# Kernel optimization log

Hardware: AMD Instinct MI355X
Metric: run time of the kernel (lower is better)

The kernel has to match this reference:

```python
import jax, jax.numpy as jnp
import numpy as np

THETA = 10000.0

def _rope_cos_sin(seq_len, head_dim, dtype=jnp.float32):
    # matches precompute_freqs_cis: freqs over even indices of head_dim
    inv = 1.0 / (THETA ** (jnp.arange(0, head_dim, 2, dtype=jnp.float32) / head_dim))  # [hd/2]
    ang = jnp.arange(seq_len, dtype=jnp.float32)[:, None] * inv[None, :]               # [S, hd/2]
    return jnp.cos(ang).astype(dtype), jnp.sin(ang).astype(dtype)

def _apply_rope(x, cos, sin):
    # x: [b, h, s, d]; pairs are interleaved (d r) with r=2 -> complex (even=real, odd=imag)
    xe = x[..., 0::2]
    xo = x[..., 1::2]
    re = xe * cos - xo * sin
    im = xe * sin + xo * cos
    # interleave back: [..., d/2, 2] -> [..., d]
    return jnp.stack([re, im], axis=-1).reshape(x.shape)

def setup_inputs() -> dict:
    key = jax.random.key(0)
    ks = jax.random.split(key, 8)
    B, S, D = 2, 2048, 1024
    s = 0.02
    return {
        "query": jax.random.normal(ks[0], (B, S, D), jnp.float32),
        "key": jax.random.normal(ks[1], (B, S, D), jnp.float32),
        "value": jax.random.normal(ks[2], (B, S, D), jnp.float32),
        "q_w": jax.random.normal(ks[3], (D, D), jnp.float32) * s,
        "q_b": jnp.zeros((D,), jnp.float32),
        "k_w": jax.random.normal(ks[4], (D, D), jnp.float32) * s,
        "k_b": jnp.zeros((D,), jnp.float32),
        "v_w": jax.random.normal(ks[5], (D, D), jnp.float32) * s,
        "v_b": jnp.zeros((D,), jnp.float32),
        "o_w": jax.random.normal(ks[6], (D, D), jnp.float32) * s,
        "o_b": jnp.zeros((D,), jnp.float32),
    }

def reference(query, key, value, q_w, q_b, k_w, k_b, v_w, v_b, o_w, o_b):
    H = 16
    B, S, D = query.shape
    hd = D // H
    scaling = hd ** -0.5

    def split_heads(x):  # [b, s, (h d)] -> [b, h, s, d]
        return x.reshape(B, -1, H, hd).transpose(0, 2, 1, 3)

    q = split_heads(query @ q_w.T + q_b)
    k = split_heads(key @ k_w.T + k_b)
    v = split_heads(value @ v_w.T + v_b)

    cos, sin = _rope_cos_sin(S, hd)
    q = _apply_rope(q, cos, sin)
    k = _apply_rope(k, cos, sin)

    scores = jnp.einsum('bhqd,bhkd->bhqk', q, k) * scaling  # [B,H,S,S]
    attn = jax.nn.softmax(scores, axis=-1)
    out = jnp.einsum('bhqk,bhkd->bhqd', attn, v)            # [B,H,S,hd]
    out = out.transpose(0, 2, 1, 3).reshape(B, S, D)
    return out @ o_w.T + o_b
```

## Files before the change

### kernel.cpp

```cpp
#include <hip/hip_runtime.h>
#include <math.h>

#define B_  2
#define S_  2048
#define D_  1024
#define H_  16
#define HD_ 64
#define M_  (B_*S_)

typedef __attribute__((ext_vector_type(8))) short bf16x8;
typedef __attribute__((ext_vector_type(4))) float f32x4;
typedef unsigned short ushort_t;

#define MFMA32 __builtin_amdgcn_mfma_f32_16x16x32_bf16

__device__ inline unsigned short f2bf(float x) {
    unsigned u = __float_as_uint(x);
    unsigned r = (u + 0x7fff + ((u >> 16) & 1)) >> 16;
    return (unsigned short)r;
}
__device__ inline void gload16(const ushort_t* g, ushort_t* l) {
    __builtin_amdgcn_global_load_lds(
        (const __attribute__((address_space(1))) unsigned*)g,
        (__attribute__((address_space(3))) unsigned*)l, 16, 0, 0);
}

__global__ __launch_bounds__(256) void prep(
    const float* __restrict__ qa, const float* __restrict__ ka,
    const float* __restrict__ va,
    const float* __restrict__ qw, const float* __restrict__ kw,
    const float* __restrict__ vw, const float* __restrict__ ow,
    ushort_t* __restrict__ qab, ushort_t* __restrict__ kab,
    ushort_t* __restrict__ vab,
    ushort_t* __restrict__ qwb, ushort_t* __restrict__ kwb,
    ushort_t* __restrict__ vwb, ushort_t* __restrict__ owb,
    float* __restrict__ cost, float* __restrict__ sint)
{
    const int z = blockIdx.y;
    const int i = blockIdx.x * 256 + threadIdx.x;
    if (z == 7) {
        if (blockIdx.x >= (S_ * 32) / 256) return;
        int s = i >> 5, w = i & 31;
        double inv = pow(10000.0, -((double)(2 * w) / (double)HD_));
        double ang = (double)s * inv;
        cost[i] = (float)cos(ang);
        sint[i] = (float)sin(ang);
        return;
    }
    const float* in;
    ushort_t* dst;
    int n4;
    switch (z) {
        case 0: in = qa; dst = qab; n4 = (M_ * D_) / 4; break;
        case 1: in = ka; dst = kab; n4 = (M_ * D_) / 4; break;
        case 2: in = va; dst = vab; n4 = (M_ * D_) / 4; break;
        case 3: in = qw; dst = qwb; n4 = (D_ * D_) / 4; break;
        case 4: in = kw; dst = kwb; n4 = (D_ * D_) / 4; break;
        case 5: in = vw; dst = vwb; n4 = (D_ * D_) / 4; break;
        default: in = ow; dst = owb; n4 = (D_ * D_) / 4; break;
    }
    if (i >= n4) return;
    float4 v = ((const float4*)in)[i];
    unsigned short h0 = f2bf(v.x), h1 = f2bf(v.y), h2 = f2bf(v.z), h3 = f2bf(v.w);
    ((uint2*)dst)[i] = make_uint2((unsigned)h0 | ((unsigned)h1 << 16),
                                  (unsigned)h2 | ((unsigned)h3 << 16));
}

__global__ __launch_bounds__(256, 3) void fused_qkv(
    const ushort_t* __restrict__ A0, const ushort_t* __restrict__ A1,
    const ushort_t* __restrict__ A2,
    const ushort_t* __restrict__ W0, const ushort_t* __restrict__ W1,
    const ushort_t* __restrict__ W2,
    const float* __restrict__ b0, const float* __restrict__ b1,
    const float* __restrict__ b2,
    ushort_t* __restrict__ O0, ushort_t* __restrict__ O1,
    ushort_t* __restrict__ O2,
    const float* __restrict__ cost, const float* __restrict__ sint)
{
    __shared__ ushort_t Ab[12288];
    __shared__ ushort_t Wb[12288];

    const int tid  = threadIdx.x;
    const int wq   = tid >> 6;
    const int lane = tid & 63;
    const int l16  = lane & 15;
    const int quad = lane >> 4;
    const int bm   = blockIdx.y * 128;
    const int bn   = blockIdx.x * 128;
    const int z    = blockIdx.z;

    const ushort_t* A = z == 0 ? A0 : z == 1 ? A1 : A2;
    const ushort_t* W = z == 0 ? W0 : z == 1 ? W1 : W2;
    const float* bias = z == 0 ? b0 : z == 1 ? b1 : b2;

    const int m16 = tid & 15;
    const int akq = (tid >> 4) & 3;
    const int tw  = tid >> 6;

    const ushort_t* gA0 = A + (size_t)(bm + tw * 16 + m16) * D_ + akq * 8;
    const ushort_t* gA1 = gA0 + (size_t)64 * D_;
    const ushort_t* gW0 = W + (size_t)(bn + tw * 16 + m16) * D_ + akq * 8;
    const ushort_t* gW1 = gW0 + (size_t)64 * D_;

    const int wm = wq >> 1, wn = wq & 1;

    f32x4 acc[4][4];
#pragma unroll
    for (int mt = 0; mt < 4; ++mt)
#pragma unroll
        for (int nt = 0; nt < 4; ++nt)
            acc[mt][nt] = (f32x4){0.f, 0.f, 0.f, 0.f};

    gload16(gA0,      &Ab[tw * 512]);
    gload16(gA1,      &Ab[(tw + 4) * 512]);
    gload16(gW0,      &Wb[tw * 512]);
    gload16(gW1,      &Wb[(tw + 4) * 512]);
    gload16(gA0 + 32, &Ab[4096 + tw * 512]);
    gload16(gA1 + 32, &Ab[4096 + (tw + 4) * 512]);
    gload16(gW0 + 32, &Wb[4096 + tw * 512]);
    gload16(gW1 + 32, &Wb[4096 + (tw + 4) * 512]);

    int bcur = 0;
    for (int k = 0; k < 32; ++k) {
        if (k < 30) {
            int bnx = bcur + 2; if (bnx >= 3) bnx -= 3;
            int ko = (k + 2) * 32;
            gload16(gA0 + ko, &Ab[bnx * 4096 + tw * 512]);
            gload16(gA1 + ko, &Ab[bnx * 4096 + (tw + 4) * 512]);
            gload16(gW0 + ko, &Wb[bnx * 4096 + tw * 512]);
            gload16(gW1 + ko, &Wb[bnx * 4096 + (tw + 4) * 512]);
            asm volatile("s_waitcnt vmcnt(8)" ::: "memory");
        } else if (k == 30) {
            asm volatile("s_waitcnt vmcnt(4)" ::: "memory");
        } else {
            asm volatile("s_waitcnt vmcnt(0)" ::: "memory");
        }
        __builtin_amdgcn_s_barrier();
        __builtin_amdgcn_sched_barrier(0);

        const ushort_t* Abc = &Ab[bcur * 4096];
        const ushort_t* Wbc = &Wb[bcur * 4096];

        bf16x8 af[4], wf[4];
#pragma unroll
        for (int mt = 0; mt < 4; ++mt)
            af[mt] = *(const bf16x8*)&Abc[(wm * 4 + mt) * 512 + lane * 8];
#pragma unroll
        for (int nt = 0; nt < 4; ++nt)
            wf[nt] = *(const bf16x8*)&Wbc[(wn * 4 + nt) * 512 + lane * 8];
#pragma unroll
        for (int mt = 0; mt < 4; ++mt)
#pragma unroll
            for (int nt = 0; nt < 4; ++nt)
                acc[mt][nt] = MFMA32(af[mt], wf[nt], acc[mt][nt], 0, 0, 0);

        __builtin_amdgcn_sched_barrier(0);
        __builtin_amdgcn_s_barrier();
        bcur += 1; if (bcur >= 3) bcur -= 3;
    }

    if (z == 0) {
        const float scale = 0.18033688011112042f;
#pragma unroll
        for (int mt = 0; mt < 4; ++mt) {
            int m = bm + wm * 64 + mt * 16 + quad * 4;
#pragma unroll
            for (int nt = 0; nt < 4; ++nt) {
                int n = bn + wn * 64 + nt * 16 + l16;
                float bb = bias[n];
                int h = n >> 6, d = n & 63, p = d >> 1;
#pragma unroll
                for (int r = 0; r < 4; ++r) {
                    int mm = m + r;
                    int s = mm & (S_ - 1), b = mm >> 11;
                    float x = acc[mt][nt][r] + bb;
                    float cs = cost[s * 32 + p], sn = sint[s * 32 + p];
                    float part = __shfl_xor(x, 1);
                    float y = (d & 1) ? (part * sn + x * cs)
                                      : (x * cs - part * sn);
                    O0[((size_t)(b * H_ + h) * S_ + s) * HD_ + d] = f2bf(y * scale);
                }
            }
        }
    } else if (z == 1) {
#pragma unroll
        for (int mt = 0; mt < 4; ++mt) {
            int m = bm + wm * 64 + mt * 16 + quad * 4;
#pragma unroll
            for (int nt = 0; nt < 4; ++nt) {
                int n = bn + wn * 64 + nt * 16 + l16;
                float bb = bias[n];
                int h = n >> 6, d = n & 63, p = d >> 1;
                int sub = ((d >> 5) & 1);
                int dq  = (d >> 3) & 3;
                int dj  = d & 7;
#pragma unroll
                for (int r = 0; r < 4; ++r) {
                    int mm = m + r;
                    int s = mm & (S_ - 1), b = mm >> 11;
                    float x = acc[mt][nt][r] + bb;
                    float cs = cost[s * 32 + p], sn = sint[s * 32 + p];
                    float part = __shfl_xor(x, 1);
                    float y = (d & 1) ? (part * sn + x * cs)
                                      : (x * cs - part * sn);
                    int kt  = s >> 5;
                    int st  = ((s >> 4) & 1) * 2 + sub;
                    size_t idx = ((size_t)(b * H_ + h) * 64 + kt) * 2048
                               + st * 512 + dq * 128 + (s & 15) * 8 + dj;
                    O1[idx] = f2bf(y);
                }
            }
        }
    } else {
#pragma unroll
        for (int mt = 0; mt < 4; ++mt) {
            int m = bm + wm * 64 + mt * 16 + quad * 4;
            int b = m >> 11, s0 = m & (S_ - 1);
            int vt = s0 >> 5;
            int kk = s0 & 31;
            int qd = (kk & 15) >> 2;
            int w0 = ((kk >> 4) & 1) * 4;
#pragma unroll
            for (int nt = 0; nt < 4; ++nt) {
                int n = bn + wn * 64 + nt * 16 + l16;
                float bb = bias[n];
                int h = n >> 6, d = n & 63;
                int mtv = d >> 4, dd = d & 15;
                unsigned short hh[4];
#pragma unroll
                for (int r = 0; r < 4; ++r)
                    hh[r] = f2bf(acc[mt][nt][r] + bb);
                size_t idx = ((size_t)(b * H_ + h) * 64 + vt) * 2048
                           + mtv * 512 + qd * 128 + dd * 8 + w0;
                *(uint2*)(O2 + idx) = make_uint2(
                    (unsigned)hh[0] | ((unsigned)hh[1] << 16),
                    (unsigned)hh[2] | ((unsigned)hh[3] << 16));
            }
        }
    }
}

__global__ __launch_bounds__(256, 2) void proj_o(
    const ushort_t* __restrict__ A, const ushort_t* __restrict__ W,
    const float* __restrict__ bias, float* __restrict__ outf)
{
    __shared__ ushort_t Ab[6144];
    __shared__ ushort_t Wb[12288];

    const int tid  = threadIdx.x;
    const int wq   = tid >> 6;
    const int lane = tid & 63;
    const int l16  = lane & 15;
    const int quad = lane >> 4;
    const int bm   = blockIdx.y * 64;
    const int bn   = blockIdx.x * 128;

    const int m16 = tid & 15;
    const int akq = (tid >> 4) & 3;
    const int tw  = tid >> 6;

    const ushort_t* gA  = A + (size_t)(bm + tw * 16 + m16) * D_ + akq * 8;
    const ushort_t* gW0 = W + (size_t)(bn + tw * 16 + m16) * D_ + akq * 8;
    const ushort_t* gW1 = gW0 + (size_t)64 * D_;

    const int wm = wq >> 1, wn = wq & 1;

    f32x4 acc[2][4];
#pragma unroll
    for (int mt = 0; mt < 2; ++mt)
#pragma unroll
        for (int nt = 0; nt < 4; ++nt)
            acc[mt][nt] = (f32x4){0.f, 0.f, 0.f, 0.f};

    gload16(gA,       &Ab[tw * 512]);
    gload16(gW0,      &Wb[tw * 512]);
    gload16(gW1,      &Wb[(tw + 4) * 512]);
    gload16(gA + 32,  &Ab[2048 + tw * 512]);
    gload16(gW0 + 32, &Wb[4096 + tw * 512]);
    gload16(gW1 + 32, &Wb[4096 + (tw + 4) * 512]);

    int bcur = 0;
    for (int k = 0; k < 32; ++k) {
        if (k < 30) {
            int bnx = bcur + 2; if (bnx >= 3) bnx -= 3;
            int ko = (k + 2) * 32;
            gload16(gA  + ko, &Ab[bnx * 2048 + tw * 512]);
            gload16(gW0 + ko, &Wb[bnx * 4096 + tw * 512]);
            gload16(gW1 + ko, &Wb[bnx * 4096 + (tw + 4) * 512]);
            asm volatile("s_waitcnt vmcnt(6)" ::: "memory");
        } else if (k == 30) {
            asm volatile("s_waitcnt vmcnt(3)" ::: "memory");
        } else {
            asm volatile("s_waitcnt vmcnt(0)" ::: "memory");
        }
        __builtin_amdgcn_s_barrier();
        __builtin_amdgcn_sched_barrier(0);

        const ushort_t* Abc = &Ab[bcur * 2048];
        const ushort_t* Wbc = &Wb[bcur * 4096];

        bf16x8 af[2], wf[4];
#pragma unroll
        for (int mt = 0; mt < 2; ++mt)
            af[mt] = *(const bf16x8*)&Abc[(wm * 2 + mt) * 512 + lane * 8];
#pragma unroll
        for (int nt = 0; nt < 4; ++nt)
            wf[nt] = *(const bf16x8*)&Wbc[(wn * 4 + nt) * 512 + lane * 8];
#pragma unroll
        for (int mt = 0; mt < 2; ++mt)
#pragma unroll
            for (int nt = 0; nt < 4; ++nt)
                acc[mt][nt] = MFMA32(af[mt], wf[nt], acc[mt][nt], 0, 0, 0);

        __builtin_amdgcn_sched_barrier(0);
        __builtin_amdgcn_s_barrier();
        bcur += 1; if (bcur >= 3) bcur -= 3;
    }

#pragma unroll
    for (int mt = 0; mt < 2; ++mt) {
        int m = bm + wm * 32 + mt * 16 + quad * 4;
#pragma unroll
        for (int nt = 0; nt < 4; ++nt) {
            int n = bn + wn * 64 + nt * 16 + l16;
            float bb = bias[n];
#pragma unroll
            for (int r = 0; r < 4; ++r)
                outf[(size_t)(m + r) * D_ + n] = acc[mt][nt][r] + bb;
        }
    }
}

__global__ __launch_bounds__(256, 2) void attn_mfma(
    const ushort_t* __restrict__ Q, const ushort_t* __restrict__ Kf,
    const ushort_t* __restrict__ Vf, ushort_t* __restrict__ AO)
{
    __shared__ __align__(16) unsigned char SM[33280 + 512];
    ushort_t* KS  = (ushort_t*)SM;
    ushort_t* VS  = (ushort_t*)(SM + 16384);
    float*    MRG = (float*)SM;
    float*    PSB = (float*)(SM + 33280);

    const int tid  = threadIdx.x;
    const int wq   = tid >> 6;
    const int lane = tid & 63;
    const int l16  = lane & 15;
    const int quad = lane >> 4;
    const int qg   = wq & 1;
    const int ks   = wq >> 1;
    const int bh   = blockIdx.y;
    const int q0   = blockIdx.x * 128 + qg * 64;

    bf16x8 qa[4][2];
#pragma unroll
    for (int nh = 0; nh < 4; ++nh)
#pragma unroll
        for (int c = 0; c < 2; ++c) {
            int row = q0 + nh * 16 + l16;
            qa[nh][c] = *(const bf16x8*)(Q + ((size_t)bh * S_ + row) * HD_
                                           + c * 32 + quad * 8);
        }
#pragma unroll
    for (int nh = 0; nh < 4; ++nh)
#pragma unroll
        for (int c = 0; c < 2; ++c)
            asm volatile("" : "+v"(qa[nh][c]));

    f32x4 oacc[4][4];
    f32x4 osum[4];
#pragma unroll
    for (int nh = 0; nh < 4; ++nh) {
        osum[nh] = (f32x4){0.f, 0.f, 0.f, 0.f};
#pragma unroll
        for (int mt = 0; mt < 4; ++mt)
            oacc[nh][mt] = (f32x4){0.f, 0.f, 0.f, 0.f};
    }

    const bf16x8 ones8 = {(short)0x3F80, (short)0x3F80, (short)0x3F80,
                          (short)0x3F80, (short)0x3F80, (short)0x3F80,
                          (short)0x3F80, (short)0x3F80};

    const ushort_t* Kbase = Kf + (size_t)bh * 64 * 2048;
    const ushort_t* Vbase = Vf + (size_t)bh * 64 * 2048;

    gload16(Kbase + tid * 8,        KS + tid * 8);
    gload16(Kbase + 2048 + tid * 8, KS + 2048 + tid * 8);
    gload16(Vbase + tid * 8,        VS + tid * 8);
    gload16(Vbase + 2048 + tid * 8, VS + 2048 + tid * 8);

    for (int i = 0; i < 32; ++i) {
        const int cur = i & 1;
        if (i < 31) {
            const int nb = cur ^ 1;
            const ushort_t* Kq = Kbase + (size_t)(i + 1) * 4096;
            const ushort_t* Vq = Vbase + (size_t)(i + 1) * 4096;
            gload16(Kq + tid * 8,        KS + nb * 4096 + tid * 8);
            gload16(Kq + 2048 + tid * 8, KS + nb * 4096 + 2048 + tid * 8);
            gload16(Vq + tid * 8,        VS + nb * 4096 + tid * 8);
            gload16(Vq + 2048 + tid * 8, VS + nb * 4096 + 2048 + tid * 8);
            asm volatile("s_waitcnt vmcnt(4)" ::: "memory");
        } else {
            asm volatile("s_waitcnt vmcnt(0)" ::: "memory");
        }
        __builtin_amdgcn_s_barrier();
        __builtin_amdgcn_sched_barrier(0);

        const ushort_t* Kc = KS + cur * 4096 + ks * 2048;
        const ushort_t* Vc = VS + cur * 4096 + ks * 2048;

        bf16x8 kf[2][2];
#pragma unroll
        for (int g = 0; g < 2; ++g)
#pragma unroll
            for (int c = 0; c < 2; ++c)
                kf[g][c] = *(const bf16x8*)&Kc[(g * 2 + c) * 512 + lane * 8];

        f32x4 s[4][2];
#pragma unroll
        for (int nh = 0; nh < 4; ++nh)
#pragma unroll
            for (int g = 0; g < 2; ++g)
                s[nh][g] = (f32x4){0.f, 0.f, 0.f, 0.f};
        __builtin_amdgcn_s_setprio(1);
#pragma unroll
        for (int c = 0; c < 2; ++c)
#pragma unroll
            for (int nh = 0; nh < 4; ++nh)
#pragma unroll
                for (int g = 0; g < 2; ++g)
                    s[nh][g] = MFMA32(kf[g][c], qa[nh][c], s[nh][g], 0, 0, 0);
        __builtin_amdgcn_s_setprio(0);

        bf16x8 pb8[4];
#pragma unroll
        for (int nh = 0; nh < 4; ++nh) {
            float p00 = __builtin_exp2f(s[nh][0][0]);
            float p01 = __builtin_exp2f(s[nh][0][1]);
            float p02 = __builtin_exp2f(s[nh][0][2]);
            float p03 = __builtin_exp2f(s[nh][0][3]);
            float p10 = __builtin_exp2f(s[nh][1][0]);
            float p11 = __builtin_exp2f(s[nh][1][1]);
            float p12 = __builtin_exp2f(s[nh][1][2]);
            float p13 = __builtin_exp2f(s[nh][1][3]);
            union { bf16x8 v; unsigned u[4]; } t;
            t.u[0] = __builtin_amdgcn_perm(__float_as_uint(p01),
                                           __float_as_uint(p00), 0x07060302);
            t.u[1] = __builtin_amdgcn_perm(__float_as_uint(p03),
                                           __float_as_uint(p02), 0x07060302);
            t.u[2] = __builtin_amdgcn_perm(__float_as_uint(p11),
                                           __float_as_uint(p10), 0x07060302);
            t.u[3] = __builtin_amdgcn_perm(__float_as_uint(p13),
                                           __float_as_uint(p12), 0x07060302);
            pb8[nh] = t.v;
        }

        __builtin_amdgcn_s_setprio(1);
#pragma unroll
        for (int mt = 0; mt < 4; ++mt) {
            bf16x8 vv = *(const bf16x8*)&Vc[mt * 512 + lane * 8];
#pragma unroll
            for (int nh = 0; nh < 4; ++nh)
                oacc[nh][mt] = MFMA32(vv, pb8[nh], oacc[nh][mt], 0, 0, 0);
        }
#pragma unroll
        for (int nh = 0; nh < 4; ++nh)
            osum[nh] = MFMA32(ones8, pb8[nh], osum[nh], 0, 0, 0);
        __builtin_amdgcn_s_setprio(0);

        __builtin_amdgcn_sched_barrier(0);
        __builtin_amdgcn_s_barrier();
    }

    if (ks == 1) {
#pragma unroll
        for (int nh = 0; nh < 4; ++nh) {
#pragma unroll
            for (int mt = 0; mt < 4; ++mt)
#pragma unroll
                for (int r = 0; r < 4; ++r)
                    MRG[(qg * 64 + nh * 16 + l16) * 65 + mt * 16 + quad * 4 + r]
                        = oacc[nh][mt][r];
            if (quad == 0)
                PSB[qg * 64 + nh * 16 + l16] = osum[nh][0];
        }
    }
    __syncthreads();
    if (ks == 0) {
        const int b = bh >> 4, h = bh & 15;
#pragma unroll
        for (int nh = 0; nh < 4; ++nh) {
            float pst = osum[nh][0] + PSB[qg * 64 + nh * 16 + l16];
            float inv = 1.0f / pst;
            int q = q0 + nh * 16 + l16;
#pragma unroll
            for (int mt = 0; mt < 4; ++mt) {
                unsigned short hh[4];
#pragma unroll
                for (int r = 0; r < 4; ++r) {
                    float x = oacc[nh][mt][r]
                        + MRG[(qg * 64 + nh * 16 + l16) * 65 + mt * 16 + quad * 4 + r];
                    hh[r] = f2bf(x * inv);
                }
                size_t base = ((size_t)b * S_ + q) * D_ + h * HD_
                            + mt * 16 + quad * 4;
                *(uint2*)(AO + base) = make_uint2(
                    (unsigned)hh[0] | ((unsigned)hh[1] << 16),
                    (unsigned)hh[2] | ((unsigned)hh[3] << 16));
            }
        }
    }
}

extern "C" void kernel_launch(void* const* d_in, const int* in_sizes, int n_in,
                              void* d_out, int out_size, void* d_ws, size_t ws_size,
                              hipStream_t stream) {
    const float* query = (const float*)d_in[0];
    const float* key   = (const float*)d_in[1];
    const float* value = (const float*)d_in[2];
    const float* q_w   = (const float*)d_in[3];
    const float* q_b   = (const float*)d_in[4];
    const float* k_w   = (const float*)d_in[5];
    const float* k_b   = (const float*)d_in[6];
    const float* v_w   = (const float*)d_in[7];
    const float* v_b   = (const float*)d_in[8];
    const float* o_w   = (const float*)d_in[9];
    const float* o_b   = (const float*)d_in[10];
    float* out = (float*)d_out;

    const size_t NT = (size_t)M_ * D_;
    const size_t WT = (size_t)D_ * D_;
    ushort_t* p = (ushort_t*)d_ws;
    ushort_t* qa_b = p; p += NT;
    ushort_t* ka_b = p; p += NT;
    ushort_t* va_b = p; p += NT;
    ushort_t* wqb  = p; p += WT;
    ushort_t* wkb  = p; p += WT;
    ushort_t* wvb  = p; p += WT;
    ushort_t* wob  = p; p += WT;
    ushort_t* Qb   = p; p += NT;
    ushort_t* Kfr  = p; p += NT;
    ushort_t* Vfr  = p; p += NT;
    ushort_t* AO   = p; p += NT;
    float* cost = (float*)p;
    float* sint = cost + (size_t)S_ * 32;

    dim3 gp((unsigned)(NT / 4 / 256), 8);
    prep<<<gp, 256, 0, stream>>>(query, key, value, q_w, k_w, v_w, o_w,
                                 qa_b, ka_b, va_b, wqb, wkb, wvb, wob,
                                 cost, sint);

    dim3 gq(D_ / 128, M_ / 128, 3);
    fused_qkv<<<gq, 256, 0, stream>>>(
        qa_b, ka_b, va_b, wqb, wkb, wvb,
        q_b, k_b, v_b, Qb, Kfr, Vfr, cost, sint);

    dim3 agrid(S_ / 128, B_ * H_);
    attn_mfma<<<agrid, 256, 0, stream>>>(Qb, Kfr, Vfr, AO);

    dim3 go(D_ / 128, M_ / 64);
    proj_o<<<go, 256, 0, stream>>>(AO, wob, o_b, out);
}
```

Before: 251.3 us.

## Remap blocks across XCDs and move to single-barrier multi-stage pipelines

Block indices in the QKV projection, output projection and attention kernels are remapped so that neighbouring tiles, which share A/W rows or the same head's K/V, land on the same XCD and can reuse its L2. The GEMM loops now issue next-stage loads after a single top-of-loop wait and barrier instead of two barriers per iteration. The attention kernel goes from a double-buffered to a triple-buffered K/V ring, prefetching two tiles ahead. This uses more shared memory in attention, which could reduce occupancy, and the remapping assumes that blocks are dispatched round-robin across XCDs.

```diff
diff --git a/kernel.cpp b/kernel.cpp
--- a/kernel.cpp
+++ b/kernel.cpp
@@ -85,9 +85,14 @@
     const int lane = tid & 63;
     const int l16  = lane & 15;
     const int quad = lane >> 4;
-    const int bm   = blockIdx.y * 128;
-    const int bn   = blockIdx.x * 128;
-    const int z    = blockIdx.z;
+
+    const unsigned flat = blockIdx.x + (blockIdx.y << 3) + (blockIdx.z << 8);
+    const unsigned xcd  = flat & 7;
+    const unsigned slot = flat >> 3;
+    const int z   = (int)(slot >> 5);
+    const unsigned rr = slot & 31;
+    const int bm  = (int)(xcd * 4 + (rr >> 3)) * 128;
+    const int bn  = (int)(rr & 7) * 128;
 
     const ushort_t* A = z == 0 ? A0 : z == 1 ? A1 : A2;
     const ushort_t* W = z == 0 ? W0 : z == 1 ? W1 : W2;
@@ -122,6 +127,15 @@
 
     int bcur = 0;
     for (int k = 0; k < 32; ++k) {
+        if (k < 31) {
+            asm volatile("s_waitcnt vmcnt(4)" ::: "memory");
+        } else {
+            asm volatile("s_waitcnt vmcnt(0)" ::: "memory");
+        }
+        __builtin_amdgcn_sched_barrier(0);
+        __builtin_amdgcn_s_barrier();
+        __builtin_amdgcn_sched_barrier(0);
+
         if (k < 30) {
             int bnx = bcur + 2; if (bnx >= 3) bnx -= 3;
             int ko = (k + 2) * 32;
@@ -129,14 +143,7 @@
             gload16(gA1 + ko, &Ab[bnx * 4096 + (tw + 4) * 512]);
             gload16(gW0 + ko, &Wb[bnx * 4096 + tw * 512]);
             gload16(gW1 + ko, &Wb[bnx * 4096 + (tw + 4) * 512]);
-            asm volatile("s_waitcnt vmcnt(8)" ::: "memory");
-        } else if (k == 30) {
-            asm volatile("s_waitcnt vmcnt(4)" ::: "memory");
-        } else {
-            asm volatile("s_waitcnt vmcnt(0)" ::: "memory");
-        }
-        __builtin_amdgcn_s_barrier();
-        __builtin_amdgcn_sched_barrier(0);
+        }
 
         const ushort_t* Abc = &Ab[bcur * 4096];
         const ushort_t* Wbc = &Wb[bcur * 4096];
@@ -154,8 +161,6 @@
             for (int nt = 0; nt < 4; ++nt)
                 acc[mt][nt] = MFMA32(af[mt], wf[nt], acc[mt][nt], 0, 0, 0);
 
-        __builtin_amdgcn_sched_barrier(0);
-        __builtin_amdgcn_s_barrier();
         bcur += 1; if (bcur >= 3) bcur -= 3;
     }
 
@@ -252,8 +257,12 @@
     const int lane = tid & 63;
     const int l16  = lane & 15;
     const int quad = lane >> 4;
-    const int bm   = blockIdx.y * 64;
-    const int bn   = blockIdx.x * 128;
+
+    const unsigned flat = blockIdx.x + (blockIdx.y << 3);
+    const unsigned xcd  = flat & 7;
+    const unsigned slot = flat >> 3;
+    const int bm = (int)(xcd * 8 + (slot >> 3)) * 64;
+    const int bn = (int)(slot & 7) * 128;
 
     const int m16 = tid & 15;
     const int akq = (tid >> 4) & 3;
@@ -281,20 +290,22 @@
 
     int bcur = 0;
     for (int k = 0; k < 32; ++k) {
+        if (k < 31) {
+            asm volatile("s_waitcnt vmcnt(3)" ::: "memory");
+        } else {
+            asm volatile("s_waitcnt vmcnt(0)" ::: "memory");
+        }
+        __builtin_amdgcn_sched_barrier(0);
+        __builtin_amdgcn_s_barrier();
+        __builtin_amdgcn_sched_barrier(0);
+
         if (k < 30) {
             int bnx = bcur + 2; if (bnx >= 3) bnx -= 3;
             int ko = (k + 2) * 32;
             gload16(gA  + ko, &Ab[bnx * 2048 + tw * 512]);
             gload16(gW0 + ko, &Wb[bnx * 4096 + tw * 512]);
             gload16(gW1 + ko, &Wb[bnx * 4096 + (tw + 4) * 512]);
-            asm volatile("s_waitcnt vmcnt(6)" ::: "memory");
-        } else if (k == 30) {
-            asm volatile("s_waitcnt vmcnt(3)" ::: "memory");
-        } else {
-            asm volatile("s_waitcnt vmcnt(0)" ::: "memory");
-        }
-        __builtin_amdgcn_s_barrier();
-        __builtin_amdgcn_sched_barrier(0);
+        }
 
         const ushort_t* Abc = &Ab[bcur * 2048];
         const ushort_t* Wbc = &Wb[bcur * 4096];
@@ -312,8 +323,6 @@
             for (int nt = 0; nt < 4; ++nt)
                 acc[mt][nt] = MFMA32(af[mt], wf[nt], acc[mt][nt], 0, 0, 0);
 
-        __builtin_amdgcn_sched_barrier(0);
-        __builtin_amdgcn_s_barrier();
         bcur += 1; if (bcur >= 3) bcur -= 3;
     }
 
@@ -335,11 +344,9 @@
     const ushort_t* __restrict__ Q, const ushort_t* __restrict__ Kf,
     const ushort_t* __restrict__ Vf, ushort_t* __restrict__ AO)
 {
-    __shared__ __align__(16) unsigned char SM[33280 + 512];
-    ushort_t* KS  = (ushort_t*)SM;
-    ushort_t* VS  = (ushort_t*)(SM + 16384);
-    float*    MRG = (float*)SM;
-    float*    PSB = (float*)(SM + 33280);
+    __shared__ __align__(16) unsigned char SM[49152 + 512];
+    float* MRG = (float*)SM;
+    float* PSB = (float*)(SM + 49152);
 
     const int tid  = threadIdx.x;
     const int wq   = tid >> 6;
@@ -348,8 +355,12 @@
     const int quad = lane >> 4;
     const int qg   = wq & 1;
     const int ks   = wq >> 1;
-    const int bh   = blockIdx.y;
-    const int q0   = blockIdx.x * 128 + qg * 64;
+
+    const unsigned flat = blockIdx.x + (blockIdx.y << 4);
+    const unsigned xcd  = flat & 7;
+    const unsigned slot = flat >> 3;
+    const int bh   = (int)(xcd * 4 + (slot >> 4));
+    const int q0   = (int)(slot & 15) * 128 + qg * 64;
 
     bf16x8 qa[4][2];
 #pragma unroll
@@ -383,30 +394,43 @@
     const ushort_t* Kbase = Kf + (size_t)bh * 64 * 2048;
     const ushort_t* Vbase = Vf + (size_t)bh * 64 * 2048;
 
-    gload16(Kbase + tid * 8,        KS + tid * 8);
-    gload16(Kbase + 2048 + tid * 8, KS + 2048 + tid * 8);
-    gload16(Vbase + tid * 8,        VS + tid * 8);
-    gload16(Vbase + 2048 + tid * 8, VS + 2048 + tid * 8);
-
+#pragma unroll
+    for (int t = 0; t < 2; ++t) {
+        ushort_t* KB = (ushort_t*)(SM + t * 16384);
+        ushort_t* VB = KB + 4096;
+        const ushort_t* Kq = Kbase + (size_t)t * 4096;
+        const ushort_t* Vq = Vbase + (size_t)t * 4096;
+        gload16(Kq + tid * 8,        KB + tid * 8);
+        gload16(Kq + 2048 + tid * 8, KB + 2048 + tid * 8);
+        gload16(Vq + tid * 8,        VB + tid * 8);
+        gload16(Vq + 2048 + tid * 8, VB + 2048 + tid * 8);
+    }
+
+    int cur = 0;
     for (int i = 0; i < 32; ++i) {
-        const int cur = i & 1;
         if (i < 31) {
-            const int nb = cur ^ 1;
-            const ushort_t* Kq = Kbase + (size_t)(i + 1) * 4096;
-            const ushort_t* Vq = Vbase + (size_t)(i + 1) * 4096;
-            gload16(Kq + tid * 8,        KS + nb * 4096 + tid * 8);
-            gload16(Kq + 2048 + tid * 8, KS + nb * 4096 + 2048 + tid * 8);
-            gload16(Vq + tid * 8,        VS + nb * 4096 + tid * 8);
-            gload16(Vq + 2048 + tid * 8, VS + nb * 4096 + 2048 + tid * 8);
             asm volatile("s_waitcnt vmcnt(4)" ::: "memory");
         } else {
             asm volatile("s_waitcnt vmcnt(0)" ::: "memory");
         }
+        __builtin_amdgcn_sched_barrier(0);
         __builtin_amdgcn_s_barrier();
         __builtin_amdgcn_sched_barrier(0);
 
-        const ushort_t* Kc = KS + cur * 4096 + ks * 2048;
-        const ushort_t* Vc = VS + cur * 4096 + ks * 2048;
+        if (i < 30) {
+            int nb = cur + 2; if (nb >= 3) nb -= 3;
+            ushort_t* KB = (ushort_t*)(SM + nb * 16384);
+            ushort_t* VB = KB + 4096;
+            const ushort_t* Kq = Kbase + (size_t)(i + 2) * 4096;
+            const ushort_t* Vq = Vbase + (size_t)(i + 2) * 4096;
+            gload16(Kq + tid * 8,        KB + tid * 8);
+            gload16(Kq + 2048 + tid * 8, KB + 2048 + tid * 8);
+            gload16(Vq + tid * 8,        VB + tid * 8);
+            gload16(Vq + 2048 + tid * 8, VB + 2048 + tid * 8);
+        }
+
+        const ushort_t* Kc = (const ushort_t*)(SM + cur * 16384) + ks * 2048;
+        const ushort_t* Vc = (const ushort_t*)(SM + cur * 16384) + 4096 + ks * 2048;
 
         bf16x8 kf[2][2];
 #pragma unroll
@@ -467,9 +491,10 @@
             osum[nh] = MFMA32(ones8, pb8[nh], osum[nh], 0, 0, 0);
         __builtin_amdgcn_s_setprio(0);
 
-        __builtin_amdgcn_sched_barrier(0);
-        __builtin_amdgcn_s_barrier();
-    }
+        cur += 1; if (cur >= 3) cur -= 3;
+    }
+
+    __syncthreads();
 
     if (ks == 1) {
 #pragma unroll
```

After: 248.6 us. No clear change (-1.1%).
